# Kernel tuning notes

Measured on AMD Instinct MI355X. Metric: run time of the kernel, lower is better.

The kernel has to match this reference:

```python
import jax, jax.numpy as jnp
import numpy as np

B, T, C = 8, 1024, 768
NH = 12
HD = C // NH  # 64


def setup_inputs() -> dict:
    key = jax.random.key(0)
    k1, k2, k3 = jax.random.split(key, 3)
    x = jax.random.normal(k1, (B, T, C), dtype=jnp.float32)
    w_attn = jax.random.normal(k2, (C, 3 * C), dtype=jnp.float32) * 0.02
    b_attn = jnp.zeros((3 * C,), dtype=jnp.float32)
    w_proj = jax.random.normal(k3, (C, C), dtype=jnp.float32) * 0.02
    b_proj = jnp.zeros((C,), dtype=jnp.float32)
    return {"x": x, "w_attn": w_attn, "b_attn": b_attn, "w_proj": w_proj, "b_proj": b_proj}


def reference(x, w_attn, b_attn, w_proj, b_proj):
    Bb, Tt, Cc = x.shape
    qkv = x @ w_attn + b_attn  # [B,T,3C]
    q, k, v = jnp.split(qkv, [Cc, 2 * Cc], axis=-1)
    # [B, NH, T, HD]
    q = q.reshape(Bb, Tt, NH, HD).swapaxes(1, 2)
    k = k.reshape(Bb, Tt, NH, HD).swapaxes(1, 2)
    v = v.reshape(Bb, Tt, NH, HD).swapaxes(1, 2)
    scale = 1.0 / jnp.sqrt(jnp.asarray(HD, dtype=x.dtype))
    att = jnp.einsum("bhqd,bhkd->bhqk", q, k) * scale  # [B,NH,T,T]
    causal = jnp.tril(jnp.ones((Tt, Tt), dtype=bool))[None, None]
    att = jnp.where(causal, att, jnp.asarray(-jnp.inf, dtype=att.dtype))
    att = jax.nn.softmax(att, axis=-1)
    y = jnp.einsum("bhqk,bhkd->bhqd", att, v)  # [B,NH,T,HD]
    y = y.swapaxes(1, 2).reshape(Bb, Tt, Cc)
    return y @ w_proj + b_proj
```

## Files before the change

kernel.cpp:

```cpp
#include <hip/hip_runtime.h>
#include <cstdint>
#include <cstddef>

typedef __attribute__((ext_vector_type(8))) short short8;
typedef __attribute__((ext_vector_type(4))) float f32x4;
typedef __attribute__((ext_vector_type(4))) unsigned short u16x4;

#define ASYNC16(gp, lp) \
  __builtin_amdgcn_global_load_lds((const __attribute__((address_space(1))) unsigned int*)(gp), \
                                   (__attribute__((address_space(3))) unsigned int*)(lp), 16, 0, 0)

__device__ __forceinline__ unsigned short f2b(float f) {
  union { float f; unsigned int u; } c; c.f = f;
  unsigned int u = c.u;
  return (unsigned short)((u + 0x7fffu + ((u >> 16) & 1u)) >> 16);
}


__global__ __launch_bounds__(256) void prep(
    const float* __restrict__ x, unsigned short* __restrict__ xb,
    const float* __restrict__ w_attn, unsigned short* __restrict__ waT,
    const float* __restrict__ w_proj, unsigned short* __restrict__ wpT) {
  __shared__ unsigned short Ts[64][65];
  const int bb = blockIdx.x;
  const int tid = threadIdx.x;
  if (bb < 3072) {
    int i = (bb * 256 + tid) * 8;
    const float* px = x + i;
    short8 v;
    for (int e = 0; e < 8; ++e) ((unsigned short*)&v)[e] = f2b(px[e]);
    *(short8*)(xb + i) = v;
    return;
  }
  const float* W; unsigned short* WT; int Kd, Nd, n0, k0;
  if (bb < 3504) {
    int t = bb - 3072; W = w_attn; WT = waT; Kd = 768; Nd = 2304;
    n0 = (t % 36) * 64; k0 = (t / 36) * 64;
  } else {
    int t = bb - 3504; W = w_proj; WT = wpT; Kd = 768; Nd = 768;
    n0 = (t % 12) * 64; k0 = (t / 12) * 64;
  }
  for (int idx = tid; idx < 4096; idx += 256) {
    int lr = idx >> 6, lc = idx & 63;
    Ts[lr][lc] = f2b(W[(size_t)(k0 + lr) * Nd + n0 + lc]);
  }
  __syncthreads();
  for (int idx = tid; idx < 4096; idx += 256) {
    int nr = idx >> 6, kc = idx & 63;
    WT[(size_t)(n0 + nr) * Kd + k0 + kc] = Ts[kc][nr];
  }
}


__global__ __launch_bounds__(256, 3) void gemm_qkv(
    const unsigned short* __restrict__ A,
    const unsigned short* __restrict__ Bt,
    const float* __restrict__ bias,
    unsigned short* __restrict__ q,
    unsigned short* __restrict__ k,
    unsigned short* __restrict__ vT)
{
  __shared__ unsigned short As[3][128 * 32];
  __shared__ unsigned short Bs[3][128 * 32];
  const int tid = threadIdx.x;
  const int w = tid >> 6, lane = tid & 63;
  const int wm = w >> 1, wn = w & 1;
  const int lr = lane & 15, lq = lane >> 4;

  const int bid = blockIdx.x;
  const int xcd = bid & 7;
  const int local = bid >> 3;
  const int ty = local >> 3;
  const int tx = xcd * 8 + (local & 7);
  const int m0 = tx * 128, n0 = ty * 128;
  const f32x4 fzero = {0.f, 0.f, 0.f, 0.f};

  f32x4 acc[4][4];
  for (int i = 0; i < 4; ++i) for (int j = 0; j < 4; ++j) acc[i][j] = fzero;

  const int b0 = w * 1024, b1 = 4096 + w * 1024;
  const int e0 = (b0 >> 1) + lane * 8, e1 = (b1 >> 1) + lane * 8;
  const int r0 = e0 >> 5, c0 = e0 & 31, r1 = e1 >> 5, c1 = e1 & 31;
  const unsigned short* Arow0 = A + (size_t)(m0 + r0) * 768 + c0;
  const unsigned short* Arow1 = A + (size_t)(m0 + r1) * 768 + c1;
  const unsigned short* Brow0 = Bt + (size_t)(n0 + r0) * 768 + c0;
  const unsigned short* Brow1 = Bt + (size_t)(n0 + r1) * 768 + c1;

#define STAGE_QKV(s, bidx) do { \
    const int kq_ = (s) * 32; \
    ASYNC16(Arow0 + kq_, (char*)As[bidx] + b0); \
    ASYNC16(Arow1 + kq_, (char*)As[bidx] + b1); \
    ASYNC16(Brow0 + kq_, (char*)Bs[bidx] + b0); \
    ASYNC16(Brow1 + kq_, (char*)Bs[bidx] + b1); \
  } while (0)

  STAGE_QKV(0, 0);
  STAGE_QKV(1, 1);

  int bi = 0;
  for (int s = 0; s < 24; ++s) {
    if (s < 23) asm volatile("s_waitcnt vmcnt(4)" ::: "memory");
    else        asm volatile("s_waitcnt vmcnt(0)" ::: "memory");
    __builtin_amdgcn_s_barrier();
    __builtin_amdgcn_sched_barrier(0);
    if (s + 2 < 24) {
      int b2 = bi + 2; if (b2 >= 3) b2 -= 3;
      STAGE_QKV(s + 2, b2);
    }
    const unsigned short* asb = As[bi];
    const unsigned short* bsb = Bs[bi];
    short8 a[4], b[4];
    for (int i = 0; i < 4; ++i)
      a[i] = *(const short8*)(asb + (wm * 64 + i * 16 + lr) * 32 + lq * 8);
    for (int j = 0; j < 4; ++j)
      b[j] = *(const short8*)(bsb + (wn * 64 + j * 16 + lr) * 32 + lq * 8);
    for (int i = 0; i < 4; ++i)
      for (int j = 0; j < 4; ++j)
        acc[i][j] = __builtin_amdgcn_mfma_f32_16x16x32_bf16(a[i], b[j], acc[i][j], 0, 0, 0);
    ++bi; if (bi == 3) bi = 0;
  }
#undef STAGE_QKV

  const int colbase = n0 + wn * 64;
  const int sec = colbase / 768;
  const float QSCALE = 0.18033688011112042f;
  for (int j = 0; j < 4; ++j) {
    int col = colbase + j * 16 + lr;
    int cc = col - sec * 768;
    int h = cc >> 6, d = cc & 63;
    float bv = bias[col];
    for (int i = 0; i < 4; ++i) {
      int row0 = m0 + wm * 64 + i * 16 + lq * 4;
      int bidx = row0 >> 10, t0 = row0 & 1023;
      int bh = bidx * 12 + h;
      if (sec == 0) {
        for (int r = 0; r < 4; ++r)
          q[((size_t)bh * 1024 + t0 + r) * 64 + d] = f2b((acc[i][j][r] + bv) * QSCALE);
      } else if (sec == 1) {
        for (int r = 0; r < 4; ++r)
          k[((size_t)bh * 1024 + t0 + r) * 64 + d] = f2b(acc[i][j][r] + bv);
      } else {
        u16x4 pv;
        pv[0] = f2b(acc[i][j][0] + bv);
        pv[1] = f2b(acc[i][j][1] + bv);
        pv[2] = f2b(acc[i][j][2] + bv);
        pv[3] = f2b(acc[i][j][3] + bv);
        *(u16x4*)(vT + ((size_t)bh * 64 + d) * 1024 + t0) = pv;
      }
    }
  }
}


__global__ __launch_bounds__(256, 3) void attn(
    const unsigned short* __restrict__ q,
    const unsigned short* __restrict__ kk,
    const unsigned short* __restrict__ vT,
    unsigned short* __restrict__ y)
{
  __shared__ unsigned short Qs[128 * 72];
  __shared__ unsigned short Ks[64 * 72];
  __shared__ unsigned short Vt[64 * 72];
  __shared__ unsigned short Ps[4 * 16 * 72];

  const int tid = threadIdx.x;
  const int w = tid >> 6, lane = tid & 63;
  const int lr = lane & 15, lq = lane >> 4;

  const int bid = blockIdx.x;
  const int xcd = bid & 7;
  const int local = bid >> 3;
  const int bh = xcd + 8 * (local >> 3);
  const int qp = local & 7;
  const int qt1 = 15 - qp;
  const int b = bh / 12, h = bh - b * 12;
  const f32x4 fzero = {0.f, 0.f, 0.f, 0.f};

  unsigned short* Pw = Ps + w * 16 * 72;
  const unsigned short* kbase = kk + (size_t)bh * 65536;
  const unsigned short* vbase = vT + (size_t)bh * 65536;

  {
    const unsigned short* qa = q + ((size_t)bh * 1024 + qp * 64) * 64;
    const unsigned short* qb = q + ((size_t)bh * 1024 + qt1 * 64) * 64;
    for (int c = tid; c < 512; c += 256) {
      int row = c >> 3, d0 = (c & 7) * 8;
      *(short8*)(Qs + row * 72 + d0)        = *(const short8*)(qa + (size_t)c * 8);
      *(short8*)(Qs + (row + 64) * 72 + d0) = *(const short8*)(qb + (size_t)c * 8);
    }
  }

  const int c0 = tid, c1 = tid + 256;
  short8 kreg[2], vreg[2];
  kreg[0] = *(const short8*)(kbase + (size_t)c0 * 8);
  kreg[1] = *(const short8*)(kbase + (size_t)c1 * 8);
  vreg[0] = *(const short8*)(vbase + (size_t)(c0 >> 3) * 1024 + (c0 & 7) * 8);
  vreg[1] = *(const short8*)(vbase + (size_t)(c1 >> 3) * 1024 + (c1 & 7) * 8);

  f32x4 o0[4], o1[4];
  float l0[4], l1[4];
  for (int jd = 0; jd < 4; ++jd) { o0[jd] = fzero; o1[jd] = fzero; }
  for (int r = 0; r < 4; ++r) { l0[r] = 0.0f; l1[r] = 0.0f; }

  const int nkt = qt1 + 1;

  for (int kt = 0; kt < nkt; ++kt) {
    __syncthreads();
    *(short8*)(Ks + (c0 >> 3) * 72 + (c0 & 7) * 8) = kreg[0];
    *(short8*)(Ks + (c1 >> 3) * 72 + (c1 & 7) * 8) = kreg[1];
    *(short8*)(Vt + (c0 >> 3) * 72 + (c0 & 7) * 8) = vreg[0];
    *(short8*)(Vt + (c1 >> 3) * 72 + (c1 & 7) * 8) = vreg[1];
    __syncthreads();
    if (kt + 1 < nkt) {
      const unsigned short* kp = kbase + (size_t)(kt + 1) * 4096;
      const unsigned short* vp = vbase + (size_t)(kt + 1) * 64;
      kreg[0] = *(const short8*)(kp + (size_t)c0 * 8);
      kreg[1] = *(const short8*)(kp + (size_t)c1 * 8);
      vreg[0] = *(const short8*)(vp + (size_t)(c0 >> 3) * 1024 + (c0 & 7) * 8);
      vreg[1] = *(const short8*)(vp + (size_t)(c1 >> 3) * 1024 + (c1 & 7) * 8);
    }

    short8 bk[2][4];
    for (int ks = 0; ks < 2; ++ks)
      for (int j = 0; j < 4; ++j)
        bk[ks][j] = *(const short8*)(Ks + (j * 16 + lr) * 72 + ks * 32 + lq * 8);

    if (kt <= qp) {
      f32x4 s[4];
      for (int j = 0; j < 4; ++j) s[j] = fzero;
      for (int ks = 0; ks < 2; ++ks) {
        short8 aq = *(const short8*)(Qs + (w * 16 + lr) * 72 + ks * 32 + lq * 8);
        for (int j = 0; j < 4; ++j)
          s[j] = __builtin_amdgcn_mfma_f32_16x16x32_bf16(aq, bk[ks][j], s[j], 0, 0, 0);
      }
      if (kt == qp) {
        int rowt = w * 16 + lq * 4;
        for (int j = 0; j < 4; ++j) {
          int colt = j * 16 + lr;
          for (int r = 0; r < 4; ++r)
            if (colt > rowt + r) s[j][r] = -1e30f;
        }
      }
      for (int r = 0; r < 4; ++r) {
        int prow = (lq * 4 + r) * 72;
        float acc = 0.0f;
        for (int j = 0; j < 4; ++j) {
          float p = __builtin_amdgcn_exp2f(s[j][r]);
          acc += p;
          union { float f; unsigned int u; } cv; cv.f = p;
          Pw[prow + j * 16 + lr] = (unsigned short)((cv.u + 0x8000u) >> 16);
        }
        l0[r] += acc;
      }
      for (int ks = 0; ks < 2; ++ks) {
        short8 ap = *(const short8*)(Pw + lr * 72 + ks * 32 + lq * 8);
        short8 bv[4];
        for (int jd = 0; jd < 4; ++jd)
          bv[jd] = *(const short8*)(Vt + (jd * 16 + lr) * 72 + ks * 32 + lq * 8);
        for (int jd = 0; jd < 4; ++jd)
          o0[jd] = __builtin_amdgcn_mfma_f32_16x16x32_bf16(ap, bv[jd], o0[jd], 0, 0, 0);
      }
    }

    {
      f32x4 s[4];
      for (int j = 0; j < 4; ++j) s[j] = fzero;
      for (int ks = 0; ks < 2; ++ks) {
        short8 aq = *(const short8*)(Qs + (64 + w * 16 + lr) * 72 + ks * 32 + lq * 8);
        for (int j = 0; j < 4; ++j)
          s[j] = __builtin_amdgcn_mfma_f32_16x16x32_bf16(aq, bk[ks][j], s[j], 0, 0, 0);
      }
      if (kt == qt1) {
        int rowt = w * 16 + lq * 4;
        for (int j = 0; j < 4; ++j) {
          int colt = j * 16 + lr;
          for (int r = 0; r < 4; ++r)
            if (colt > rowt + r) s[j][r] = -1e30f;
        }
      }
      for (int r = 0; r < 4; ++r) {
        int prow = (lq * 4 + r) * 72;
        float acc = 0.0f;
        for (int j = 0; j < 4; ++j) {
          float p = __builtin_amdgcn_exp2f(s[j][r]);
          acc += p;
          union { float f; unsigned int u; } cv; cv.f = p;
          Pw[prow + j * 16 + lr] = (unsigned short)((cv.u + 0x8000u) >> 16);
        }
        l1[r] += acc;
      }
      for (int ks = 0; ks < 2; ++ks) {
        short8 ap = *(const short8*)(Pw + lr * 72 + ks * 32 + lq * 8);
        short8 bv[4];
        for (int jd = 0; jd < 4; ++jd)
          bv[jd] = *(const short8*)(Vt + (jd * 16 + lr) * 72 + ks * 32 + lq * 8);
        for (int jd = 0; jd < 4; ++jd)
          o1[jd] = __builtin_amdgcn_mfma_f32_16x16x32_bf16(ap, bv[jd], o1[jd], 0, 0, 0);
      }
    }
  }

  for (int r = 0; r < 4; ++r) {
    float a0 = l0[r], a1 = l1[r];
    for (int off = 1; off < 16; off <<= 1) {
      a0 += __shfl_xor(a0, off, 16);
      a1 += __shfl_xor(a1, off, 16);
    }
    l0[r] = 1.0f / a0;
    l1[r] = 1.0f / a1;
  }
  int t0 = qp * 64 + w * 16 + lq * 4;
  int t1 = qt1 * 64 + w * 16 + lq * 4;
  for (int jd = 0; jd < 4; ++jd) {
    int d = jd * 16 + lr;
    for (int r = 0; r < 4; ++r) {
      y[((size_t)b * 1024 + t0 + r) * 768 + h * 64 + d] = f2b(o0[jd][r] * l0[r]);
      y[((size_t)b * 1024 + t1 + r) * 768 + h * 64 + d] = f2b(o1[jd][r] * l1[r]);
    }
  }
}


__global__ __launch_bounds__(256, 4) void gemm_proj(
    const unsigned short* __restrict__ A,
    const unsigned short* __restrict__ Bt,
    const float* __restrict__ bias,
    float* __restrict__ out)
{
  __shared__ unsigned short As[3][64 * 32];
  __shared__ unsigned short Bs[3][128 * 32];
  const int tid = threadIdx.x;
  const int w = tid >> 6, lane = tid & 63;
  const int wm = w >> 1, wn = w & 1;
  const int lr = lane & 15, lq = lane >> 4;

  const int bid = blockIdx.x;
  const int xcd = bid & 7;
  const int local = bid >> 3;
  const int ty = local >> 4;
  const int tx = xcd * 16 + (local & 15);
  const int m0 = tx * 64, n0 = ty * 128;
  const f32x4 fzero = {0.f, 0.f, 0.f, 0.f};

  f32x4 acc[2][4];
  for (int i = 0; i < 2; ++i) for (int j = 0; j < 4; ++j) acc[i][j] = fzero;

  const int ba = w * 1024;
  const int ea = (ba >> 1) + lane * 8;
  const int ar = ea >> 5, ac = ea & 31;
  const int b0 = w * 1024, b1 = 4096 + w * 1024;
  const int e0 = (b0 >> 1) + lane * 8, e1 = (b1 >> 1) + lane * 8;
  const int r0 = e0 >> 5, c0 = e0 & 31, r1 = e1 >> 5, c1 = e1 & 31;
  const unsigned short* Arow  = A + (size_t)(m0 + ar) * 768 + ac;
  const unsigned short* Brow0 = Bt + (size_t)(n0 + r0) * 768 + c0;
  const unsigned short* Brow1 = Bt + (size_t)(n0 + r1) * 768 + c1;

#define STAGE_PROJ(s, bidx) do { \
    const int kq_ = (s) * 32; \
    ASYNC16(Arow  + kq_, (char*)As[bidx] + ba); \
    ASYNC16(Brow0 + kq_, (char*)Bs[bidx] + b0); \
    ASYNC16(Brow1 + kq_, (char*)Bs[bidx] + b1); \
  } while (0)

  STAGE_PROJ(0, 0);
  STAGE_PROJ(1, 1);

  int bi = 0;
  for (int s = 0; s < 24; ++s) {
    if (s < 23) asm volatile("s_waitcnt vmcnt(3)" ::: "memory");
    else        asm volatile("s_waitcnt vmcnt(0)" ::: "memory");
    __builtin_amdgcn_s_barrier();
    __builtin_amdgcn_sched_barrier(0);
    if (s + 2 < 24) {
      int b2 = bi + 2; if (b2 >= 3) b2 -= 3;
      STAGE_PROJ(s + 2, b2);
    }
    const unsigned short* asb = As[bi];
    const unsigned short* bsb = Bs[bi];
    short8 a[2], b[4];
    for (int i = 0; i < 2; ++i)
      a[i] = *(const short8*)(asb + (wm * 32 + i * 16 + lr) * 32 + lq * 8);
    for (int j = 0; j < 4; ++j)
      b[j] = *(const short8*)(bsb + (wn * 64 + j * 16 + lr) * 32 + lq * 8);
    for (int i = 0; i < 2; ++i)
      for (int j = 0; j < 4; ++j)
        acc[i][j] = __builtin_amdgcn_mfma_f32_16x16x32_bf16(a[i], b[j], acc[i][j], 0, 0, 0);
    ++bi; if (bi == 3) bi = 0;
  }
#undef STAGE_PROJ

  for (int j = 0; j < 4; ++j) {
    int col = n0 + wn * 64 + j * 16 + lr;
    float bv = bias[col];
    for (int i = 0; i < 2; ++i) {
      int row0 = m0 + wm * 32 + i * 16 + lq * 4;
      for (int r = 0; r < 4; ++r)
        out[(size_t)(row0 + r) * 768 + col] = acc[i][j][r] + bv;
    }
  }
}


extern "C" void kernel_launch(void* const* d_in, const int* in_sizes, int n_in,
                              void* d_out, int out_size, void* d_ws, size_t ws_size,
                              hipStream_t stream) {
  const float* x      = (const float*)d_in[0];
  const float* w_attn = (const float*)d_in[1];
  const float* b_attn = (const float*)d_in[2];
  const float* w_proj = (const float*)d_in[3];
  const float* b_proj = (const float*)d_in[4];
  float* out = (float*)d_out;

  char* p = (char*)d_ws;
  unsigned short* xb  = (unsigned short*)p; p += (size_t)8192 * 768 * 2;
  unsigned short* waT = (unsigned short*)p; p += (size_t)2304 * 768 * 2;
  unsigned short* wpT = (unsigned short*)p; p += (size_t)768 * 768 * 2;
  unsigned short* qb  = (unsigned short*)p; p += (size_t)96 * 1024 * 64 * 2;
  unsigned short* kb  = (unsigned short*)p; p += (size_t)96 * 1024 * 64 * 2;
  unsigned short* vTb = (unsigned short*)p; p += (size_t)96 * 64 * 1024 * 2;
  unsigned short* yb  = (unsigned short*)p; p += (size_t)8192 * 768 * 2;

  prep<<<3648, 256, 0, stream>>>(x, xb, w_attn, waT, w_proj, wpT);
  gemm_qkv<<<1152, 256, 0, stream>>>(xb, waT, b_attn, qb, kb, vTb);
  attn<<<768, 256, 0, stream>>>(qb, kb, vTb, yb);
  gemm_proj<<<768, 256, 0, stream>>>(yb, wpT, b_proj, out);
}
```

Before: 190.1 us.

## Use K=64 double-buffered XOR-swizzled LDS tiles in QKV and projection GEMMs

```diff
diff --git a/kernel.cpp b/kernel.cpp
--- a/kernel.cpp
+++ b/kernel.cpp
@@ -52,7 +52,7 @@
 }
 
 
-__global__ __launch_bounds__(256, 3) void gemm_qkv(
+__global__ __launch_bounds__(256, 2) void gemm_qkv(
     const unsigned short* __restrict__ A,
     const unsigned short* __restrict__ Bt,
     const float* __restrict__ bias,
@@ -60,8 +60,8 @@
     unsigned short* __restrict__ k,
     unsigned short* __restrict__ vT)
 {
-  __shared__ unsigned short As[3][128 * 32];
-  __shared__ unsigned short Bs[3][128 * 32];
+  __shared__ unsigned short As[2][128 * 64];
+  __shared__ unsigned short Bs[2][128 * 64];
   const int tid = threadIdx.x;
   const int w = tid >> 6, lane = tid & 63;
   const int wm = w >> 1, wn = w & 1;
@@ -78,46 +78,54 @@
   f32x4 acc[4][4];
   for (int i = 0; i < 4; ++i) for (int j = 0; j < 4; ++j) acc[i][j] = fzero;
 
-  const int b0 = w * 1024, b1 = 4096 + w * 1024;
-  const int e0 = (b0 >> 1) + lane * 8, e1 = (b1 >> 1) + lane * 8;
-  const int r0 = e0 >> 5, c0 = e0 & 31, r1 = e1 >> 5, c1 = e1 & 31;
-  const unsigned short* Arow0 = A + (size_t)(m0 + r0) * 768 + c0;
-  const unsigned short* Arow1 = A + (size_t)(m0 + r1) * 768 + c1;
-  const unsigned short* Brow0 = Bt + (size_t)(n0 + r0) * 768 + c0;
-  const unsigned short* Brow1 = Bt + (size_t)(n0 + r1) * 768 + c1;
+  const int trow = tid >> 3;
+  const int tcol = (tid & 7) ^ (trow & 7);
+  const unsigned short* Asrc = A + (size_t)(m0 + trow) * 768 + tcol * 8;
+  const unsigned short* Bsrc = Bt + (size_t)(n0 + trow) * 768 + tcol * 8;
+  const int dst0 = tid * 16;
 
 #define STAGE_QKV(s, bidx) do { \
-    const int kq_ = (s) * 32; \
-    ASYNC16(Arow0 + kq_, (char*)As[bidx] + b0); \
-    ASYNC16(Arow1 + kq_, (char*)As[bidx] + b1); \
-    ASYNC16(Brow0 + kq_, (char*)Bs[bidx] + b0); \
-    ASYNC16(Brow1 + kq_, (char*)Bs[bidx] + b1); \
+    const unsigned short* as_ = Asrc + (s) * 64; \
+    const unsigned short* bs_ = Bsrc + (s) * 64; \
+    ASYNC16(as_,            (char*)As[bidx] + dst0); \
+    ASYNC16(as_ + 32 * 768, (char*)As[bidx] + dst0 + 4096); \
+    ASYNC16(as_ + 64 * 768, (char*)As[bidx] + dst0 + 8192); \
+    ASYNC16(as_ + 96 * 768, (char*)As[bidx] + dst0 + 12288); \
+    ASYNC16(bs_,            (char*)Bs[bidx] + dst0); \
+    ASYNC16(bs_ + 32 * 768, (char*)Bs[bidx] + dst0 + 4096); \
+    ASYNC16(bs_ + 64 * 768, (char*)Bs[bidx] + dst0 + 8192); \
+    ASYNC16(bs_ + 96 * 768, (char*)Bs[bidx] + dst0 + 12288); \
   } while (0)
 
   STAGE_QKV(0, 0);
-  STAGE_QKV(1, 1);
-
-  int bi = 0;
-  for (int s = 0; s < 24; ++s) {
-    if (s < 23) asm volatile("s_waitcnt vmcnt(4)" ::: "memory");
-    else        asm volatile("s_waitcnt vmcnt(0)" ::: "memory");
+
+  const int swz = (lq ^ (lr & 7)) * 16;
+  const int arow = (wm * 64 + lr) * 128;
+  const int brow = (wn * 64 + lr) * 128;
+
+  for (int s = 0; s < 12; ++s) {
+    __builtin_amdgcn_s_barrier();
+    if (s + 1 < 12) {
+      STAGE_QKV(s + 1, (s + 1) & 1);
+      asm volatile("s_waitcnt vmcnt(8)" ::: "memory");
+    } else {
+      asm volatile("s_waitcnt vmcnt(0)" ::: "memory");
+    }
     __builtin_amdgcn_s_barrier();
     __builtin_amdgcn_sched_barrier(0);
-    if (s + 2 < 24) {
-      int b2 = bi + 2; if (b2 >= 3) b2 -= 3;
-      STAGE_QKV(s + 2, b2);
-    }
-    const unsigned short* asb = As[bi];
-    const unsigned short* bsb = Bs[bi];
-    short8 a[4], b[4];
-    for (int i = 0; i < 4; ++i)
-      a[i] = *(const short8*)(asb + (wm * 64 + i * 16 + lr) * 32 + lq * 8);
-    for (int j = 0; j < 4; ++j)
-      b[j] = *(const short8*)(bsb + (wn * 64 + j * 16 + lr) * 32 + lq * 8);
-    for (int i = 0; i < 4; ++i)
+    const char* asb = (const char*)As[s & 1];
+    const char* bsb = (const char*)Bs[s & 1];
+    for (int ks = 0; ks < 2; ++ks) {
+      const int cb = swz ^ (ks << 6);
+      short8 a[4], b[4];
+      for (int i = 0; i < 4; ++i)
+        a[i] = *(const short8*)(asb + arow + i * 2048 + cb);
       for (int j = 0; j < 4; ++j)
-        acc[i][j] = __builtin_amdgcn_mfma_f32_16x16x32_bf16(a[i], b[j], acc[i][j], 0, 0, 0);
-    ++bi; if (bi == 3) bi = 0;
+        b[j] = *(const short8*)(bsb + brow + j * 2048 + cb);
+      for (int i = 0; i < 4; ++i)
+        for (int j = 0; j < 4; ++j)
+          acc[i][j] = __builtin_amdgcn_mfma_f32_16x16x32_bf16(a[i], b[j], acc[i][j], 0, 0, 0);
+    }
   }
 #undef STAGE_QKV
 
@@ -321,14 +329,14 @@
 }
 
 
-__global__ __launch_bounds__(256, 4) void gemm_proj(
+__global__ __launch_bounds__(256, 3) void gemm_proj(
     const unsigned short* __restrict__ A,
     const unsigned short* __restrict__ Bt,
     const float* __restrict__ bias,
     float* __restrict__ out)
 {
-  __shared__ unsigned short As[3][64 * 32];
-  __shared__ unsigned short Bs[3][128 * 32];
+  __shared__ unsigned short As[2][64 * 64];
+  __shared__ unsigned short Bs[2][128 * 64];
   const int tid = threadIdx.x;
   const int w = tid >> 6, lane = tid & 63;
   const int wm = w >> 1, wn = w & 1;
@@ -345,47 +353,52 @@
   f32x4 acc[2][4];
   for (int i = 0; i < 2; ++i) for (int j = 0; j < 4; ++j) acc[i][j] = fzero;
 
-  const int ba = w * 1024;
-  const int ea = (ba >> 1) + lane * 8;
-  const int ar = ea >> 5, ac = ea & 31;
-  const int b0 = w * 1024, b1 = 4096 + w * 1024;
-  const int e0 = (b0 >> 1) + lane * 8, e1 = (b1 >> 1) + lane * 8;
-  const int r0 = e0 >> 5, c0 = e0 & 31, r1 = e1 >> 5, c1 = e1 & 31;
-  const unsigned short* Arow  = A + (size_t)(m0 + ar) * 768 + ac;
-  const unsigned short* Brow0 = Bt + (size_t)(n0 + r0) * 768 + c0;
-  const unsigned short* Brow1 = Bt + (size_t)(n0 + r1) * 768 + c1;
+  const int trow = tid >> 3;
+  const int tcol = (tid & 7) ^ (trow & 7);
+  const unsigned short* Asrc = A + (size_t)(m0 + trow) * 768 + tcol * 8;
+  const unsigned short* Bsrc = Bt + (size_t)(n0 + trow) * 768 + tcol * 8;
+  const int dst0 = tid * 16;
 
 #define STAGE_PROJ(s, bidx) do { \
-    const int kq_ = (s) * 32; \
-    ASYNC16(Arow  + kq_, (char*)As[bidx] + ba); \
-    ASYNC16(Brow0 + kq_, (char*)Bs[bidx] + b0); \
-    ASYNC16(Brow1 + kq_, (char*)Bs[bidx] + b1); \
+    const unsigned short* as_ = Asrc + (s) * 64; \
+    const unsigned short* bs_ = Bsrc + (s) * 64; \
+    ASYNC16(as_,            (char*)As[bidx] + dst0); \
+    ASYNC16(as_ + 32 * 768, (char*)As[bidx] + dst0 + 4096); \
+    ASYNC16(bs_,            (char*)Bs[bidx] + dst0); \
+    ASYNC16(bs_ + 32 * 768, (char*)Bs[bidx] + dst0 + 4096); \
+    ASYNC16(bs_ + 64 * 768, (char*)Bs[bidx] + dst0 + 8192); \
+    ASYNC16(bs_ + 96 * 768, (char*)Bs[bidx] + dst0 + 12288); \
   } while (0)
 
   STAGE_PROJ(0, 0);
-  STAGE_PROJ(1, 1);
-
-  int bi = 0;
-  for (int s = 0; s < 24; ++s) {
-    if (s < 23) asm volatile("s_waitcnt vmcnt(3)" ::: "memory");
-    else        asm volatile("s_waitcnt vmcnt(0)" ::: "memory");
+
+  const int swz = (lq ^ (lr & 7)) * 16;
+  const int arow = (wm * 32 + lr) * 128;
+  const int brow = (wn * 64 + lr) * 128;
+
+  for (int s = 0; s < 12; ++s) {
+    __builtin_amdgcn_s_barrier();
+    if (s + 1 < 12) {
+      STAGE_PROJ(s + 1, (s + 1) & 1);
+      asm volatile("s_waitcnt vmcnt(6)" ::: "memory");
+    } else {
+      asm volatile("s_waitcnt vmcnt(0)" ::: "memory");
+    }
     __builtin_amdgcn_s_barrier();
     __builtin_amdgcn_sched_barrier(0);
-    if (s + 2 < 24) {
-      int b2 = bi + 2; if (b2 >= 3) b2 -= 3;
-      STAGE_PROJ(s + 2, b2);
-    }
-    const unsigned short* asb = As[bi];
-    const unsigned short* bsb = Bs[bi];
-    short8 a[2], b[4];
-    for (int i = 0; i < 2; ++i)
-      a[i] = *(const short8*)(asb + (wm * 32 + i * 16 + lr) * 32 + lq * 8);
-    for (int j = 0; j < 4; ++j)
-      b[j] = *(const short8*)(bsb + (wn * 64 + j * 16 + lr) * 32 + lq * 8);
-    for (int i = 0; i < 2; ++i)
+    const char* asb = (const char*)As[s & 1];
+    const char* bsb = (const char*)Bs[s & 1];
+    for (int ks = 0; ks < 2; ++ks) {
+      const int cb = swz ^ (ks << 6);
+      short8 a[2], b[4];
+      for (int i = 0; i < 2; ++i)
+        a[i] = *(const short8*)(asb + arow + i * 2048 + cb);
       for (int j = 0; j < 4; ++j)
-        acc[i][j] = __builtin_amdgcn_mfma_f32_16x16x32_bf16(a[i], b[j], acc[i][j], 0, 0, 0);
-    ++bi; if (bi == 3) bi = 0;
+        b[j] = *(const short8*)(bsb + brow + j * 2048 + cb);
+      for (int i = 0; i < 2; ++i)
+        for (int j = 0; j < 4; ++j)
+          acc[i][j] = __builtin_amdgcn_mfma_f32_16x16x32_bf16(a[i], b[j], acc[i][j], 0, 0, 0);
+    }
   }
 #undef STAGE_PROJ
 
```

After: 174.1 us. 8.4% less time.
